# Optimization experiments

Measured on AMD Instinct MI355X. Metric: run time of the kernel, lower is better.

## Reference

```python
import jax, jax.numpy as jnp
import numpy as np


def setup_inputs() -> dict:
    key = jax.random.key(0)
    ks = jax.random.split(key, 6)
    B, T, C, NL = 2, 2048, 2048, 512
    s = 0.02
    return {
        "x": jax.random.normal(ks[0], (B, T, C), jnp.float32),
        "W_dq": jax.random.normal(ks[1], (NL, C), jnp.float32) * s,
        "W_dkv": jax.random.normal(ks[2], (NL, C), jnp.float32) * s,
        "W_uk": jax.random.normal(ks[3], (C, NL), jnp.float32) * s,
        "W_uv": jax.random.normal(ks[4], (C, NL), jnp.float32) * s,
        "W_o": jax.random.normal(ks[5], (C, C), jnp.float32) * s,
        "n_head": 16,
    }


def reference(x, W_dq, W_dkv, W_uk, W_uv, W_o, n_head):
    B, T, C = x.shape
    nl = W_dkv.shape[0]
    nh = n_head
    hs = C // nh
    # Absorbed key projection: (W_dq^T @ W_uk^T @ W_uk) -> [C, nl] -> [nh, hs, nl]
    k_abs = (W_dq.T @ W_uk.T @ W_uk).reshape(nh, hs, nl)
    # Absorbed value/output projection: (W_uv^T @ W_o^T) -> [nl, C] -> [nh, nl, hs]
    v_abs = jnp.transpose((W_uv.T @ W_o.T).reshape(nl, nh, hs), (1, 0, 2))
    # Latent KV cache: [B, T, nl]
    c_kv = x @ W_dkv.T
    # Queries: raw x split into heads (matches reference: no W_dq/W_uq applied to q)
    q = x.reshape(B, T, nh, hs).transpose(0, 2, 1, 3)  # [B, nh, T, hs]
    # Scores via chained low-rank matmuls: q @ k_abs @ c_kv^T
    scores = jnp.einsum('bhtd,hdl,bsl->bhts', q, k_abs, c_kv) / jnp.sqrt(
        jnp.asarray(hs, x.dtype))
    # Causal mask + softmax (dropout p=0 -> identity)
    mask = jnp.tril(jnp.ones((T, T), dtype=bool))
    scores = jnp.where(mask, scores, -jnp.inf)
    attn = jax.nn.softmax(scores, axis=-1)  # [B, nh, T, T]
    # Output: attn @ c_kv @ v_abs
    y = jnp.einsum('bhts,bsl,hld->bhtd', attn, c_kv, v_abs)  # [B, nh, T, hs]
    y = y.transpose(0, 2, 1, 3).reshape(B, T, C)
    return (y, c_kv)
```

## Files before the change

kernel.cpp:

```cpp
#include <hip/hip_runtime.h>
#include <stdint.h>

typedef __attribute__((ext_vector_type(8))) short short8;
typedef __attribute__((ext_vector_type(4))) short short4v;
typedef __attribute__((ext_vector_type(2))) short short2v;
typedef __attribute__((ext_vector_type(4))) float f32x4;
typedef __attribute__((ext_vector_type(8))) __bf16 bf16x8;

__device__ __forceinline__ short f2bf(float f) {
  unsigned u = __builtin_bit_cast(unsigned, f);
  u = (u + 0x7FFFu + ((u >> 16) & 1u)) >> 16;
  return (short)u;
}

__device__ __forceinline__ short f2bf_fast(float f) {
  return (short)((__builtin_bit_cast(unsigned, f) + 0x8000u) >> 16);
}

__device__ __forceinline__ f32x4 mfma16(short8 a, short8 b, f32x4 c) {
  return __builtin_amdgcn_mfma_f32_16x16x32_bf16(
      __builtin_bit_cast(bf16x8, a), __builtin_bit_cast(bf16x8, b), c, 0, 0, 0);
}

__device__ __forceinline__ void gload_lds16(const void* g, void* l) {
  __builtin_amdgcn_global_load_lds(
      (const __attribute__((address_space(1))) unsigned int*)g,
      (__attribute__((address_space(3))) unsigned int*)l, 16, 0, 0);
}

__global__ __launch_bounds__(256) void conv3(
    const float* __restrict__ x, const float* __restrict__ wdkv,
    const float* __restrict__ wo,
    short* __restrict__ xb, short* __restrict__ wdkvb, short* __restrict__ wob) {
  int i = blockIdx.x * 256 + threadIdx.x;
  const float* in; short* out; int off;
  if (i < 2097152)      { in = x;    out = xb;    off = i; }
  else if (i < 2359296) { in = wdkv; out = wdkvb; off = i - 2097152; }
  else                  { in = wo;   out = wob;   off = i - 2359296; }
  f32x4 v = ((const f32x4*)in)[off];
  short4v o;
  o[0] = f2bf(v[0]); o[1] = f2bf(v[1]); o[2] = f2bf(v[2]); o[3] = f2bf(v[3]);
  ((short4v*)out)[off] = o;
}

__global__ __launch_bounds__(256) void trans_w3(
    const float* __restrict__ Wuk, const float* __restrict__ Wdq,
    const float* __restrict__ Wuv,
    short* __restrict__ wukT, short* __restrict__ wdqT, short* __restrict__ wuvT)
{
  const int z = blockIdx.y;
  const float* in; short* out; int R, C;
  if (z == 0)      { in = Wuk; out = wukT; R = 2048; C = 512; }
  else if (z == 1) { in = Wdq; out = wdqT; R = 512;  C = 2048; }
  else             { in = Wuv; out = wuvT; R = 2048; C = 512; }
  const int tpc = C >> 6;
  const int r0 = (blockIdx.x / tpc) << 6, c0 = (blockIdx.x % tpc) << 6;
  __shared__ float tile[64][65];
  const int tid = threadIdx.x;
#pragma unroll
  for (int i = 0; i < 4; ++i) {
    int idx = tid + i * 256;
    int row = idx >> 4, col4 = (idx & 15) * 4;
    f32x4 v = *(const f32x4*)(in + (size_t)(r0 + row) * C + c0 + col4);
    tile[row][col4] = v[0]; tile[row][col4 + 1] = v[1];
    tile[row][col4 + 2] = v[2]; tile[row][col4 + 3] = v[3];
  }
  __syncthreads();
#pragma unroll
  for (int i = 0; i < 4; ++i) {
    int idx = tid + i * 256;
    int crow = idx >> 4, r4 = (idx & 15) * 4;
    short4v o;
    o[0] = f2bf(tile[r4][crow]);     o[1] = f2bf(tile[r4 + 1][crow]);
    o[2] = f2bf(tile[r4 + 2][crow]); o[3] = f2bf(tile[r4 + 3][crow]);
    *(short4v*)(out + (size_t)(c0 + crow) * R + r0 + r4) = o;
  }
}

__global__ __launch_bounds__(256) void trans_vabs(const short* __restrict__ in,
                                                  short* __restrict__ out) {
  const int c0 = blockIdx.x << 6, l0 = blockIdx.y << 6;
  __shared__ short tile[64][66];
  const int tid = threadIdx.x;
#pragma unroll
  for (int i = 0; i < 8; ++i) {
    int idx = tid + i * 256;
    int row = idx >> 5, col2 = (idx & 31) * 2;
    short2v v = *(const short2v*)(in + (size_t)(l0 + row) * 2048 + c0 + col2);
    tile[row][col2] = v[0]; tile[row][col2 + 1] = v[1];
  }
  __syncthreads();
  const int h = c0 >> 7, d0 = c0 & 127;
  short* ob = out + ((size_t)h << 16) + (size_t)d0 * 512 + l0;
#pragma unroll
  for (int i = 0; i < 8; ++i) {
    int idx = tid + i * 256;
    int crow = idx >> 5, l2 = (idx & 31) * 2;
    short2v v;
    v[0] = tile[l2][crow]; v[1] = tile[l2 + 1][crow];
    *(short2v*)(ob + (size_t)crow * 512 + l2) = v;
  }
}


__device__ __forceinline__ void gemm128_body(
    const short* A, const short* B, float* Cf, short* Cb,
    int K, int lda, int ldb, int ldc, int bx, int by, float scale)
{
  const int tid = threadIdx.x, wid = tid >> 6, L = tid & 63;
  const int g = L >> 4, r16 = L & 15, wr = wid >> 1, wc = wid & 1;
  const int rl = L >> 3, ru = L & 7;

  __shared__ short Asm[128 * 64], Bsm[128 * 64];
  char* Ab = (char*)Asm;
  char* Bb = (char*)Bsm;

  const f32x4 fz = {0.f, 0.f, 0.f, 0.f};
  f32x4 acc[4][4];
#pragma unroll
  for (int m = 0; m < 4; ++m)
#pragma unroll
    for (int n = 0; n < 4; ++n) acc[m][n] = fz;

  const int aRow0 = bx * 128, bRow0 = by * 128;

  for (int kt = 0; kt < K; kt += 64) {
#pragma unroll
    for (int i = 0; i < 4; ++i) {
      int row = i * 32 + wid * 8 + rl;
      gload_lds16(A + (size_t)(aRow0 + row) * lda + kt + ((ru ^ rl) * 8),
                  Ab + (i * 32 + wid * 8) * 128);
    }
#pragma unroll
    for (int i = 0; i < 4; ++i) {
      int row = i * 32 + wid * 8 + rl;
      gload_lds16(B + (size_t)(bRow0 + row) * ldb + kt + ((ru ^ rl) * 8),
                  Bb + (i * 32 + wid * 8) * 128);
    }
    __syncthreads();
#pragma unroll
    for (int kk = 0; kk < 2; ++kk) {
      short8 a[4], b2[4];
#pragma unroll
      for (int m = 0; m < 4; ++m) {
        int row = wr * 64 + m * 16 + r16;
        a[m] = *(const short8*)(Ab + row * 128 + (((kk * 4 + g) ^ (row & 7)) << 4));
      }
#pragma unroll
      for (int n = 0; n < 4; ++n) {
        int row = wc * 64 + n * 16 + r16;
        b2[n] = *(const short8*)(Bb + row * 128 + (((kk * 4 + g) ^ (row & 7)) << 4));
      }
#pragma unroll
      for (int m = 0; m < 4; ++m)
#pragma unroll
        for (int n = 0; n < 4; ++n) acc[m][n] = mfma16(a[m], b2[n], acc[m][n]);
    }
    __syncthreads();
  }

#pragma unroll
  for (int m = 0; m < 4; ++m) {
    int row0 = aRow0 + wr * 64 + m * 16 + g * 4;
#pragma unroll
    for (int n = 0; n < 4; ++n) {
      int col = bRow0 + wc * 64 + n * 16 + r16;
#pragma unroll
      for (int e = 0; e < 4; ++e) {
        long idx = (long)(row0 + e) * ldc + col;
        float v = acc[m][n][e] * scale;
        if (Cf) Cf[idx] = v;
        if (Cb) Cb[idx] = f2bf(v);
      }
    }
  }
}

__device__ __forceinline__ void gemm64_body(
    const short* A, const short* B, float* Cf, short* Cb,
    int K, int lda, int ldb, int ldc, int bx, int by, float scale)
{
  const int tid = threadIdx.x, wid = tid >> 6, L = tid & 63;
  const int g = L >> 4, r16 = L & 15, wr = wid >> 1, wc = wid & 1;

  __shared__ short Asm[64 * 64], Bsm[64 * 64];
  char* Ab = (char*)Asm;
  char* Bb = (char*)Bsm;

  const f32x4 fz = {0.f, 0.f, 0.f, 0.f};
  f32x4 acc[2][2] = {{fz, fz}, {fz, fz}};
  const int aRow0 = bx * 64, bRow0 = by * 64;

  for (int kt = 0; kt < K; kt += 64) {
#pragma unroll
    for (int i = 0; i < 2; ++i) {
      int ug = i * 256 + wid * 64;
      int row = (ug + L) >> 3, u = (ug + L) & 7;
      gload_lds16(A + (size_t)(aRow0 + row) * lda + kt + ((u ^ (row & 7)) * 8),
                  Ab + ug * 16);
    }
#pragma unroll
    for (int i = 0; i < 2; ++i) {
      int ug = i * 256 + wid * 64;
      int row = (ug + L) >> 3, u = (ug + L) & 7;
      gload_lds16(B + (size_t)(bRow0 + row) * ldb + kt + ((u ^ (row & 7)) * 8),
                  Bb + ug * 16);
    }
    __syncthreads();
#pragma unroll
    for (int kk = 0; kk < 2; ++kk) {
      short8 a[2], b2[2];
#pragma unroll
      for (int m = 0; m < 2; ++m) {
        int row = wr * 32 + m * 16 + r16;
        a[m] = *(const short8*)(Ab + row * 128 + (((kk * 4 + g) ^ (row & 7)) << 4));
      }
#pragma unroll
      for (int n = 0; n < 2; ++n) {
        int row = wc * 32 + n * 16 + r16;
        b2[n] = *(const short8*)(Bb + row * 128 + (((kk * 4 + g) ^ (row & 7)) << 4));
      }
#pragma unroll
      for (int m = 0; m < 2; ++m)
#pragma unroll
        for (int n = 0; n < 2; ++n) acc[m][n] = mfma16(a[m], b2[n], acc[m][n]);
    }
    __syncthreads();
  }

#pragma unroll
  for (int m = 0; m < 2; ++m) {
    int row0 = aRow0 + wr * 32 + m * 16 + g * 4;
#pragma unroll
    for (int n = 0; n < 2; ++n) {
      int col = bRow0 + wc * 32 + n * 16 + r16;
#pragma unroll
      for (int e = 0; e < 4; ++e) {
        long idx = (long)(row0 + e) * ldc + col;
        float v = acc[m][n][e] * scale;
        if (Cf) Cf[idx] = v;
        if (Cb) Cb[idx] = f2bf(v);
      }
    }
  }
}

__global__ __launch_bounds__(256) void gemm_jobs3(
    const short* __restrict__ wukT, const short* __restrict__ wuvT,
    const short* __restrict__ wo, const short* __restrict__ x_bf,
    const short* __restrict__ wdkv,
    short* __restrict__ m1, short* __restrict__ vflat,
    float* __restrict__ ckv_f, short* __restrict__ ckvb)
{
  const int bid = blockIdx.x;
  const short *A, *B; short* Cb; float* Cf; int bx, by, ldc;
  if (bid < 16)      { A = wukT; B = wukT; Cb = m1;    Cf = nullptr;
                       bx = bid >> 2;        by = bid & 3;         ldc = 512; }
  else if (bid < 80) { A = wuvT; B = wo;   Cb = vflat; Cf = nullptr;
                       bx = (bid - 16) >> 4; by = (bid - 16) & 15; ldc = 2048; }
  else               { A = x_bf; B = wdkv; Cb = ckvb;  Cf = ckv_f;
                       bx = (bid - 80) >> 2; by = (bid - 80) & 3;  ldc = 512; }
  gemm128_body(A, B, Cf, Cb, 2048, 2048, 2048, ldc, bx, by, 1.0f);
}

__global__ __launch_bounds__(256) void gemm_kabs(
    const short* __restrict__ wdqT, const short* __restrict__ m1,
    short* __restrict__ kabs)
{
  gemm64_body(wdqT, m1, nullptr, kabs, 512, 512, 512, 512,
              blockIdx.x, blockIdx.y, 0.08838834764831845f * 1.4426950408889634f);
}

__global__ __launch_bounds__(256) void gemm_keffveff(
    const short* __restrict__ ckvb, const short* __restrict__ kabs,
    const short* __restrict__ vabsT,
    short* __restrict__ keffT, short* __restrict__ veffT)
{
  const int bz = blockIdx.z;
  const short *A, *B; short* C; int ldc, bx, by;
  if (bz < 32) {
    int b = bz >> 4, h = bz & 15;
    A = ckvb + (size_t)b * 2048 * 512;
    B = kabs + (size_t)h * 128 * 512;
    C = keffT + (size_t)bz * 2048 * 128;
    ldc = 128; bx = blockIdx.x; by = 0;
  } else {
    int bh = bz - 32, b = bh >> 4, h = bh & 15;
    A = vabsT + (size_t)h * 128 * 512;
    B = ckvb + (size_t)b * 2048 * 512;
    C = veffT + (size_t)bh * 128 * 2048;
    ldc = 2048; bx = 0; by = blockIdx.x;
  }
  gemm128_body(A, B, nullptr, C, 512, 512, 512, ldc, bx, by, 1.0f);
}

__global__ __launch_bounds__(256) void flash_d128(
    const short* __restrict__ x_bf,
    const short* __restrict__ kT,
    const short* __restrict__ vT,
    float* __restrict__ y)
{
  const int f = blockIdx.x;
  const int r = f & 1, bh = (f >> 1) & 31, pp = f >> 6;
  const int b = bh >> 4, h = bh & 15;
  const int tid = threadIdx.x, wid = tid >> 6, L = tid & 63, g = L >> 4, r16 = L & 15;

  __shared__ char lds[73728];

  const char* kbase = (const char*)(kT + (size_t)bh * (2048 * 128));
  const char* vbase = (const char*)(vT + (size_t)bh * (128 * 2048));

  int kfo[4], vfo[2], pao[2], pwo[4];
#pragma unroll
  for (int ks = 0; ks < 4; ++ks)
    kfo[ks] = 8192 + r16 * 256 + (((ks * 4 + g) ^ r16) << 4);
#pragma unroll
  for (int kk = 0; kk < 2; ++kk) {
    vfo[kk] = 24576 + r16 * 128 + (((kk * 4 + g) ^ (r16 & 7)) << 4);
    pao[kk] = wid * 2048 + r16 * 128 + (((kk * 4 + g) ^ (r16 & 7)) << 4);
  }
#pragma unroll
  for (int e = 0; e < 4; ++e) {
    int qrow = g * 4 + e;
    pwo[e] = wid * 2048 + qrow * 128 + ((r16 * 2) ^ ((qrow & 7) << 4));
  }

  const int kLaneOff = (wid * 4 + g) * 256 + ((r16 ^ (wid * 4 + g)) << 4);
  const size_t vLaneOff = (size_t)(wid * 8 + (L >> 3)) * 4096 + (((L & 7) ^ (L >> 3)) << 4);

  short8 ones;
#pragma unroll
  for (int i = 0; i < 8; ++i) ones[i] = (short)0x3F80;
  const f32x4 fz = {0.f, 0.f, 0.f, 0.f};

  for (int seg = 0; seg < 2; ++seg) {
    const int qt = seg ? 15 - pp : pp;
    const int qw = qt * 128 + r * 64 + wid * 16;
    const int nkt = 2 * qt + 1 + r;

    short8 qf[4];
#pragma unroll
    for (int ks = 0; ks < 4; ++ks)
      qf[ks] = *(const short8*)(x_bf +
          (size_t)(b * 2048 + qw + r16) * 2048 + h * 128 + ks * 32 + g * 8);

    f32x4 acc[8];
#pragma unroll
    for (int n = 0; n < 8; ++n) acc[n] = fz;
    f32x4 acc_l = fz;

    const char* kp = kbase + kLaneOff;
    const char* vp = vbase + vLaneOff;

    auto stage = [&](int c) {
      const int base = 8192 + c * 32768 + wid * 1024;
#pragma unroll
      for (int i = 0; i < 4; ++i)
        gload_lds16(kp + i * 4096, lds + base + i * 4096);
#pragma unroll
      for (int i = 0; i < 4; ++i)
        gload_lds16(vp + (size_t)i * 131072, lds + base + 16384 + i * 4096);
      kp += 16384;
      vp += 128;
    };

    stage(0);

    for (int kt = 0; kt < nkt; ++kt) {
      const int c = kt & 1, co = c * 32768, s0 = kt * 64;

      if (kt + 1 < nkt) {
        stage(c ^ 1);
        asm volatile("s_waitcnt vmcnt(8)" ::: "memory");
      } else {
        asm volatile("s_waitcnt vmcnt(0)" ::: "memory");
      }
      __builtin_amdgcn_s_barrier();

      f32x4 s[4] = {fz, fz, fz, fz};
      __builtin_amdgcn_s_setprio(1);
#pragma unroll
      for (int ks = 0; ks < 4; ++ks) {
        const char* kb = lds + co + kfo[ks];
#pragma unroll
        for (int n = 0; n < 4; ++n)
          s[n] = mfma16(qf[ks], *(const short8*)(kb + n * 4096), s[n]);
      }
      __builtin_amdgcn_s_setprio(0);

      if (s0 + 63 > qw) {
#pragma unroll
        for (int n = 0; n < 4; ++n)
#pragma unroll
          for (int e = 0; e < 4; ++e)
            if (s0 + n * 16 + r16 > qw + g * 4 + e) s[n][e] = -3e38f;
      }

#pragma unroll
      for (int n = 0; n < 4; ++n)
#pragma unroll
        for (int e = 0; e < 4; ++e) {
          float p = exp2f(s[n][e]);
          *(short*)(lds + (pwo[e] ^ (n << 5))) = f2bf_fast(p);
        }
      short8 pa[2];
#pragma unroll
      for (int kk = 0; kk < 2; ++kk)
        pa[kk] = *(const short8*)(lds + pao[kk]);

      __builtin_amdgcn_s_setprio(1);
#pragma unroll
      for (int kk = 0; kk < 2; ++kk) acc_l = mfma16(pa[kk], ones, acc_l);
#pragma unroll
      for (int kk = 0; kk < 2; ++kk) {
        const char* vb = lds + co + vfo[kk];
#pragma unroll
        for (int n = 0; n < 8; ++n)
          acc[n] = mfma16(pa[kk], *(const short8*)(vb + n * 2048), acc[n]);
      }
      __builtin_amdgcn_s_setprio(0);

      asm volatile("s_waitcnt lgkmcnt(0)" ::: "memory");
      __builtin_amdgcn_s_barrier();
    }

    float inv[4];
#pragma unroll
    for (int e = 0; e < 4; ++e) inv[e] = 1.f / acc_l[e];
#pragma unroll
    for (int n = 0; n < 8; ++n)
#pragma unroll
      for (int e = 0; e < 4; ++e) {
        int row = qw + g * 4 + e;
        y[(size_t)(b * 2048 + row) * 2048 + h * 128 + n * 16 + r16] =
            acc[n][e] * inv[e];
      }
  }
}


extern "C" void kernel_launch(void* const* d_in, const int* in_sizes, int n_in,
                              void* d_out, int out_size, void* d_ws, size_t ws_size,
                              hipStream_t stream) {
  const float* x    = (const float*)d_in[0];
  const float* Wdq  = (const float*)d_in[1];
  const float* Wdkv = (const float*)d_in[2];
  const float* Wuk  = (const float*)d_in[3];
  const float* Wuv  = (const float*)d_in[4];
  const float* Wo   = (const float*)d_in[5];
  float* y     = (float*)d_out;
  float* ckv_f = y + (size_t)2 * 2048 * 2048;

  char* w = (char*)d_ws;
  auto alloc = [&](size_t bytes) { char* p = w; w += (bytes + 255) & ~(size_t)255; return p; };
  short* x_bf   = (short*)alloc((size_t)2 * 2048 * 2048 * 2);
  short* wdkv   = (short*)alloc((size_t)512 * 2048 * 2);
  short* wukT   = (short*)alloc((size_t)512 * 2048 * 2);
  short* wdqT   = (short*)alloc((size_t)2048 * 512 * 2);
  short* wuvT   = (short*)alloc((size_t)512 * 2048 * 2);
  short* wo     = (short*)alloc((size_t)2048 * 2048 * 2);
  short* m1     = (short*)alloc((size_t)512 * 512 * 2);
  short* kabs   = (short*)alloc((size_t)2048 * 512 * 2);
  short* vflat  = (short*)alloc((size_t)512 * 2048 * 2);
  short* vabsT  = (short*)alloc((size_t)16 * 128 * 512 * 2);
  short* ckvb   = (short*)alloc((size_t)2 * 2048 * 512 * 2);
  short* keffT  = (short*)alloc((size_t)32 * 2048 * 128 * 2);
  short* veffT  = (short*)alloc((size_t)32 * 128 * 2048 * 2);

  conv3<<<13312, 256, 0, stream>>>(x, Wdkv, Wo, x_bf, wdkv, wo);
  trans_w3<<<dim3(256, 3), 256, 0, stream>>>(Wuk, Wdq, Wuv, wukT, wdqT, wuvT);

  gemm_jobs3<<<208, 256, 0, stream>>>(wukT, wuvT, wo, x_bf, wdkv,
                                      m1, vflat, ckv_f, ckvb);
  gemm_kabs<<<dim3(32, 8), 256, 0, stream>>>(wdqT, m1, kabs);
  trans_vabs<<<dim3(32, 8), 256, 0, stream>>>(vflat, vabsT);

  gemm_keffveff<<<dim3(16, 1, 64), 256, 0, stream>>>(ckvb, kabs, vabsT, keffT, veffT);

  flash_d128<<<512, 256, 0, stream>>>(x_bf, keffT, veffT, y);
}
```

Before: 169.0 us.

## Use 64-tile GEMM for fused jobs and split flash attention into smaller KV tiles

The combined GEMM launch switches from 128x128 to 64x64 tiles, quadrupling the block count from 208 to 832 so more CUs have work. The flash kernel drops the two-segment paired scheduling and instead launches one block per 64-row query slab (1024 blocks, heaviest slabs first). It also shrinks the KV tile from 64 to 32 keys, which halves LDS use and should allow higher occupancy. The trade-off is more iterations, barriers and per-tile overhead, plus less reuse per loaded tile.

Result: faster. 157.6 us (-6.7%).

```diff
diff --git a/kernel.cpp b/kernel.cpp
--- a/kernel.cpp
+++ b/kernel.cpp
@@ -254,13 +254,13 @@
 {
   const int bid = blockIdx.x;
   const short *A, *B; short* Cb; float* Cf; int bx, by, ldc;
-  if (bid < 16)      { A = wukT; B = wukT; Cb = m1;    Cf = nullptr;
-                       bx = bid >> 2;        by = bid & 3;         ldc = 512; }
-  else if (bid < 80) { A = wuvT; B = wo;   Cb = vflat; Cf = nullptr;
-                       bx = (bid - 16) >> 4; by = (bid - 16) & 15; ldc = 2048; }
-  else               { A = x_bf; B = wdkv; Cb = ckvb;  Cf = ckv_f;
-                       bx = (bid - 80) >> 2; by = (bid - 80) & 3;  ldc = 512; }
-  gemm128_body(A, B, Cf, Cb, 2048, 2048, 2048, ldc, bx, by, 1.0f);
+  if (bid < 64)       { A = wukT; B = wukT; Cb = m1;    Cf = nullptr;
+                        bx = bid >> 3;         by = bid & 7;         ldc = 512; }
+  else if (bid < 320) { A = wuvT; B = wo;   Cb = vflat; Cf = nullptr;
+                        bx = (bid - 64) >> 5;  by = (bid - 64) & 31; ldc = 2048; }
+  else                { A = x_bf; B = wdkv; Cb = ckvb;  Cf = ckv_f;
+                        bx = (bid - 320) >> 3; by = (bid - 320) & 7; ldc = 512; }
+  gemm64_body(A, B, Cf, Cb, 2048, 2048, 2048, ldc, bx, by, 1.0f);
 }
 
 __global__ __launch_bounds__(256) void gemm_kabs(
@@ -301,141 +301,131 @@
     float* __restrict__ y)
 {
   const int f = blockIdx.x;
-  const int r = f & 1, bh = (f >> 1) & 31, pp = f >> 6;
+  const int bh = f & 31, s_ = f >> 5;
+  const int qt = 15 - (s_ >> 1), r = s_ & 1;
   const int b = bh >> 4, h = bh & 15;
   const int tid = threadIdx.x, wid = tid >> 6, L = tid & 63, g = L >> 4, r16 = L & 15;
-
-  __shared__ char lds[73728];
-
-  const char* kbase = (const char*)(kT + (size_t)bh * (2048 * 128));
-  const char* vbase = (const char*)(vT + (size_t)bh * (128 * 2048));
-
-  int kfo[4], vfo[2], pao[2], pwo[4];
+  const int qw = qt * 128 + r * 64 + wid * 16;
+  const int nkt = 4 * qt + 2 * r + 2;
+
+  __shared__ char lds[36864];
+
+  const char* kp0; const char* kp1; const char* vp0; const char* vp1;
+  {
+    const char* kbase = (const char*)(kT + (size_t)bh * (2048 * 128));
+    const char* vbase = (const char*)(vT + (size_t)bh * (128 * 2048));
+    int u0 = wid * 128 + L, u1 = u0 + 64;
+    int s0u = u0 >> 4, c0u = u0 & 15, s1u = u1 >> 4, c1u = u1 & 15;
+    kp0 = kbase + s0u * 256 + ((c0u ^ (s0u & 15)) << 4);
+    kp1 = kbase + s1u * 256 + ((c1u ^ (s1u & 15)) << 4);
+    int d0u = u0 >> 2, e0u = u0 & 3, d1u = u1 >> 2, e1u = u1 & 3;
+    vp0 = vbase + (size_t)d0u * 4096 + ((e0u ^ ((d0u >> 1) & 3)) << 4);
+    vp1 = vbase + (size_t)d1u * 4096 + ((e1u ^ ((d1u >> 1) & 3)) << 4);
+  }
+
+  int kfo[4], vfo, pao, pwo[4];
 #pragma unroll
   for (int ks = 0; ks < 4; ++ks)
-    kfo[ks] = 8192 + r16 * 256 + (((ks * 4 + g) ^ r16) << 4);
-#pragma unroll
-  for (int kk = 0; kk < 2; ++kk) {
-    vfo[kk] = 24576 + r16 * 128 + (((kk * 4 + g) ^ (r16 & 7)) << 4);
-    pao[kk] = wid * 2048 + r16 * 128 + (((kk * 4 + g) ^ (r16 & 7)) << 4);
-  }
+    kfo[ks] = 4096 + r16 * 256 + (((ks * 4 + g) ^ r16) << 4);
+  vfo = 12288 + r16 * 64 + ((g ^ ((r16 >> 1) & 3)) << 4);
+  pao = wid * 1024 + r16 * 64 + ((g ^ ((r16 >> 1) & 3)) << 4);
 #pragma unroll
   for (int e = 0; e < 4; ++e) {
-    int qrow = g * 4 + e;
-    pwo[e] = wid * 2048 + qrow * 128 + ((r16 * 2) ^ ((qrow & 7) << 4));
-  }
-
-  const int kLaneOff = (wid * 4 + g) * 256 + ((r16 ^ (wid * 4 + g)) << 4);
-  const size_t vLaneOff = (size_t)(wid * 8 + (L >> 3)) * 4096 + (((L & 7) ^ (L >> 3)) << 4);
+    int q = g * 4 + e, q13 = (q >> 1) & 3;
+    pwo[e] = wid * 1024 + q * 64 + (((r16 >> 3) ^ q13) << 4) + (r16 & 7) * 2;
+  }
+
+  short8 qf[4];
+#pragma unroll
+  for (int ks = 0; ks < 4; ++ks)
+    qf[ks] = *(const short8*)(x_bf +
+        (size_t)(b * 2048 + qw + r16) * 2048 + h * 128 + ks * 32 + g * 8);
+
+  const f32x4 fz = {0.f, 0.f, 0.f, 0.f};
+  f32x4 acc[8];
+#pragma unroll
+  for (int n = 0; n < 8; ++n) acc[n] = fz;
+  f32x4 acc_l = fz;
 
   short8 ones;
 #pragma unroll
   for (int i = 0; i < 8; ++i) ones[i] = (short)0x3F80;
-  const f32x4 fz = {0.f, 0.f, 0.f, 0.f};
-
-  for (int seg = 0; seg < 2; ++seg) {
-    const int qt = seg ? 15 - pp : pp;
-    const int qw = qt * 128 + r * 64 + wid * 16;
-    const int nkt = 2 * qt + 1 + r;
-
-    short8 qf[4];
-#pragma unroll
-    for (int ks = 0; ks < 4; ++ks)
-      qf[ks] = *(const short8*)(x_bf +
-          (size_t)(b * 2048 + qw + r16) * 2048 + h * 128 + ks * 32 + g * 8);
-
-    f32x4 acc[8];
-#pragma unroll
-    for (int n = 0; n < 8; ++n) acc[n] = fz;
-    f32x4 acc_l = fz;
-
-    const char* kp = kbase + kLaneOff;
-    const char* vp = vbase + vLaneOff;
-
-    auto stage = [&](int c) {
-      const int base = 8192 + c * 32768 + wid * 1024;
-#pragma unroll
-      for (int i = 0; i < 4; ++i)
-        gload_lds16(kp + i * 4096, lds + base + i * 4096);
-#pragma unroll
-      for (int i = 0; i < 4; ++i)
-        gload_lds16(vp + (size_t)i * 131072, lds + base + 16384 + i * 4096);
-      kp += 16384;
-      vp += 128;
-    };
-
-    stage(0);
-
-    for (int kt = 0; kt < nkt; ++kt) {
-      const int c = kt & 1, co = c * 32768, s0 = kt * 64;
-
-      if (kt + 1 < nkt) {
-        stage(c ^ 1);
-        asm volatile("s_waitcnt vmcnt(8)" ::: "memory");
-      } else {
-        asm volatile("s_waitcnt vmcnt(0)" ::: "memory");
-      }
-      __builtin_amdgcn_s_barrier();
-
-      f32x4 s[4] = {fz, fz, fz, fz};
-      __builtin_amdgcn_s_setprio(1);
-#pragma unroll
-      for (int ks = 0; ks < 4; ++ks) {
-        const char* kb = lds + co + kfo[ks];
-#pragma unroll
-        for (int n = 0; n < 4; ++n)
-          s[n] = mfma16(qf[ks], *(const short8*)(kb + n * 4096), s[n]);
-      }
-      __builtin_amdgcn_s_setprio(0);
-
-      if (s0 + 63 > qw) {
-#pragma unroll
-        for (int n = 0; n < 4; ++n)
-#pragma unroll
-          for (int e = 0; e < 4; ++e)
-            if (s0 + n * 16 + r16 > qw + g * 4 + e) s[n][e] = -3e38f;
-      }
-
-#pragma unroll
-      for (int n = 0; n < 4; ++n)
-#pragma unroll
-        for (int e = 0; e < 4; ++e) {
-          float p = exp2f(s[n][e]);
-          *(short*)(lds + (pwo[e] ^ (n << 5))) = f2bf_fast(p);
-        }
-      short8 pa[2];
-#pragma unroll
-      for (int kk = 0; kk < 2; ++kk)
-        pa[kk] = *(const short8*)(lds + pao[kk]);
-
-      __builtin_amdgcn_s_setprio(1);
-#pragma unroll
-      for (int kk = 0; kk < 2; ++kk) acc_l = mfma16(pa[kk], ones, acc_l);
-#pragma unroll
-      for (int kk = 0; kk < 2; ++kk) {
-        const char* vb = lds + co + vfo[kk];
-#pragma unroll
-        for (int n = 0; n < 8; ++n)
-          acc[n] = mfma16(pa[kk], *(const short8*)(vb + n * 2048), acc[n]);
-      }
-      __builtin_amdgcn_s_setprio(0);
-
-      asm volatile("s_waitcnt lgkmcnt(0)" ::: "memory");
-      __builtin_amdgcn_s_barrier();
-    }
-
-    float inv[4];
-#pragma unroll
-    for (int e = 0; e < 4; ++e) inv[e] = 1.f / acc_l[e];
-#pragma unroll
-    for (int n = 0; n < 8; ++n)
+
+  auto stage = [&](int c) {
+    char* dstK = lds + 4096 + c * 16384 + wid * 2048;
+    gload_lds16(kp0, dstK);
+    gload_lds16(kp1, dstK + 1024);
+    gload_lds16(vp0, dstK + 8192);
+    gload_lds16(vp1, dstK + 9216);
+    kp0 += 8192; kp1 += 8192;
+    vp0 += 64;  vp1 += 64;
+  };
+
+  stage(0);
+
+  for (int kt = 0; kt < nkt; ++kt) {
+    const int c = kt & 1, co = c * 16384, s0 = kt * 32;
+
+    if (kt + 1 < nkt) {
+      stage(c ^ 1);
+      asm volatile("s_waitcnt vmcnt(4)" ::: "memory");
+    } else {
+      asm volatile("s_waitcnt vmcnt(0)" ::: "memory");
+    }
+    __builtin_amdgcn_s_barrier();
+
+    f32x4 s[2] = {fz, fz};
+    __builtin_amdgcn_s_setprio(1);
+#pragma unroll
+    for (int ks = 0; ks < 4; ++ks) {
+      const char* kb = lds + co + kfo[ks];
+      s[0] = mfma16(qf[ks], *(const short8*)(kb), s[0]);
+      s[1] = mfma16(qf[ks], *(const short8*)(kb + 4096), s[1]);
+    }
+    __builtin_amdgcn_s_setprio(0);
+
+    if (s0 + 31 > qw) {
+#pragma unroll
+      for (int n = 0; n < 2; ++n)
+#pragma unroll
+        for (int e = 0; e < 4; ++e)
+          if (s0 + n * 16 + r16 > qw + g * 4 + e) s[n][e] = -3e38f;
+    }
+
+#pragma unroll
+    for (int n = 0; n < 2; ++n)
 #pragma unroll
       for (int e = 0; e < 4; ++e) {
-        int row = qw + g * 4 + e;
-        y[(size_t)(b * 2048 + row) * 2048 + h * 128 + n * 16 + r16] =
-            acc[n][e] * inv[e];
-      }
-  }
+        float p = exp2f(s[n][e]);
+        *(short*)(lds + (pwo[e] ^ (n << 5))) = f2bf_fast(p);
+      }
+    short8 pa = *(const short8*)(lds + pao);
+
+    __builtin_amdgcn_s_setprio(1);
+    acc_l = mfma16(pa, ones, acc_l);
+    {
+      const char* vb = lds + co + vfo;
+#pragma unroll
+      for (int n = 0; n < 8; ++n)
+        acc[n] = mfma16(pa, *(const short8*)(vb + n * 1024), acc[n]);
+    }
+    __builtin_amdgcn_s_setprio(0);
+
+    asm volatile("s_waitcnt lgkmcnt(0)" ::: "memory");
+    __builtin_amdgcn_s_barrier();
+  }
+
+  float inv[4];
+#pragma unroll
+  for (int e = 0; e < 4; ++e) inv[e] = 1.f / acc_l[e];
+#pragma unroll
+  for (int n = 0; n < 8; ++n)
+#pragma unroll
+    for (int e = 0; e < 4; ++e) {
+      int row = qw + g * 4 + e;
+      y[(size_t)(b * 2048 + row) * 2048 + h * 128 + n * 16 + r16] =
+          acc[n][e] * inv[e];
+    }
 }
 
 
@@ -470,12 +460,12 @@
   conv3<<<13312, 256, 0, stream>>>(x, Wdkv, Wo, x_bf, wdkv, wo);
   trans_w3<<<dim3(256, 3), 256, 0, stream>>>(Wuk, Wdq, Wuv, wukT, wdqT, wuvT);
 
-  gemm_jobs3<<<208, 256, 0, stream>>>(wukT, wuvT, wo, x_bf, wdkv,
+  gemm_jobs3<<<832, 256, 0, stream>>>(wukT, wuvT, wo, x_bf, wdkv,
                                       m1, vflat, ckv_f, ckvb);
   gemm_kabs<<<dim3(32, 8), 256, 0, stream>>>(wdqT, m1, kabs);
   trans_vabs<<<dim3(32, 8), 256, 0, stream>>>(vflat, vabsT);
 
   gemm_keffveff<<<dim3(16, 1, 64), 256, 0, stream>>>(ckvb, kabs, vabsT, keffT, veffT);
 
-  flash_d128<<<512, 256, 0, stream>>>(x_bf, keffT, veffT, y);
-}
+  flash_d128<<<1024, 256, 0, stream>>>(x_bf, keffT, veffT, y);
+}
```
